# Kernel tuning notes

Measured on AMD Instinct MI355X. Metric: run time of the kernel, lower is better.

## Reference

```python
import jax, jax.numpy as jnp
import numpy as np

B, L, D, K = 1024, 50, 128, 20
NI, NL, NT = 100000, 10000, 2000  # items, locs, times


def _emb(k, n, d):
    e = jax.random.normal(k, (n, d), dtype=jnp.float32) * 0.02
    return e.at[0].set(0.0)  # padding_idx=0


def setup_inputs() -> dict:
    key = jax.random.key(0)
    ks = jax.random.split(key, 40)
    inp = {}
    inp['item'] = jax.random.randint(ks[0], (B, L), 0, NI)
    inp['locs'] = jax.random.randint(ks[1], (B,), 0, NL)
    inp['times'] = jax.random.randint(ks[2], (B,), 0, NT)
    inp['session_emb'] = jax.random.normal(ks[3], (B, 1, D), dtype=jnp.float32)
    # embedding tables
    inp['loc_emb'] = _emb(ks[4], NL, D)
    inp['time_emb'] = _emb(ks[5], NT, D)
    inp['item_emb'] = _emb(ks[6], NI, D)
    # sampled fixed-fanout neighbor tables Hg[edge]['neighbor']
    inp['nb_IL'] = jax.random.randint(ks[7], (NL, K), 0, NI)   # item neighbors of locs
    inp['nb_TL'] = jax.random.randint(ks[8], (NL, K), 0, NT)   # time neighbors of locs
    inp['nb_IT'] = jax.random.randint(ks[9], (NT, K), 0, NI)   # item neighbors of times
    inp['nb_LT'] = jax.random.randint(ks[10], (NT, K), 0, NL)  # loc neighbors of times
    inp['nb_II'] = jax.random.randint(ks[11], (NI, K), 0, NI)  # item neighbors of items
    inp['nb_LI'] = jax.random.randint(ks[12], (NI, K), 0, NL)  # loc neighbors of items
    inp['nb_TI'] = jax.random.randint(ks[13], (NI, K), 0, NT)  # time neighbors of items
    # 7 HeteAggregator params: Linear(2D -> D) + ReLU
    s = 1.0 / np.sqrt(2 * D)
    names = ['IL', 'TL', 'IT', 'LT', 'II', 'LI', 'TI']
    for i, nm in enumerate(names):
        inp['W_' + nm] = jax.random.uniform(ks[14 + i], (2 * D, D), jnp.float32, -s, s)
        inp['b_' + nm] = jnp.zeros((D,), jnp.float32)
    # 3 SemanticAttention params: Linear(D->D,bias)+tanh, Linear(D->1,no bias)
    s2 = 1.0 / np.sqrt(D)
    for i, nm in enumerate(['l', 't', 'i']):
        inp['Ws_' + nm] = jax.random.uniform(ks[24 + 3 * i], (D, D), jnp.float32, -s2, s2)
        inp['bs_' + nm] = jnp.zeros((D,), jnp.float32)
        inp['q_' + nm] = jax.random.uniform(ks[25 + 3 * i], (D, 1), jnp.float32, -s2, s2)
    return inp


def hete_agg(h_self, h_neigh, W, b):
    # h_self: [N, D]; h_neigh: [N, K, D] -> mean-aggregate, concat, linear, relu
    agg = h_neigh.mean(axis=1)
    return jax.nn.relu(jnp.concatenate([h_self, agg], axis=-1) @ W + b)


def sem_att(z, Ws, bs, q):
    # HAN-style semantic attention. z: [N, M, D]
    w = jnp.tanh(z @ Ws + bs) @ q          # [N, M, 1]
    beta = jax.nn.softmax(w.mean(axis=0), axis=0)  # [M, 1]
    return (beta[None] * z).sum(axis=1)    # [N, D]


def reference(item, locs, times, session_emb,
              loc_emb, time_emb, item_emb,
              nb_IL, nb_TL, nb_IT, nb_LT, nb_II, nb_LI, nb_TI,
              W_IL, b_IL, W_TL, b_TL, W_IT, b_IT, W_LT, b_LT,
              W_II, b_II, W_LI, b_LI, W_TI, b_TI,
              Ws_l, bs_l, q_l, Ws_t, bs_t, q_t, Ws_i, bs_i, q_i):
    iids = item.reshape(-1)  # [B*L]
    h_l_IL = hete_agg(loc_emb[locs], item_emb[nb_IL[locs]], W_IL, b_IL)
    h_l_TL = hete_agg(loc_emb[locs], time_emb[nb_TL[locs]], W_TL, b_TL)
    h_t_IT = hete_agg(time_emb[times], item_emb[nb_IT[times]], W_IT, b_IT)
    h_t_LT = hete_agg(time_emb[times], loc_emb[nb_LT[times]], W_LT, b_LT)
    h_i_II = hete_agg(item_emb[iids], item_emb[nb_II[iids]], W_II, b_II)
    h_i_LI = hete_agg(item_emb[iids], loc_emb[nb_LI[iids]], W_LI, b_LI)
    h_i_TI = hete_agg(item_emb[iids], time_emb[nb_TI[iids]], W_TI, b_TI)
    h_s = session_emb.squeeze(1)  # [B, D]
    h_l_stack = jnp.stack([h_l_IL, h_l_TL, h_s], axis=1)
    h_t_stack = jnp.stack([h_t_IT, h_t_LT, h_s], axis=1)
    h_i_stack = jnp.stack([h_i_II, h_i_TI, h_i_LI], axis=1)
    h_items = sem_att(h_i_stack, Ws_i, bs_i, q_i)
    h_locs = sem_att(h_l_stack, Ws_l, bs_l, q_l)
    h_times = sem_att(h_t_stack, Ws_t, bs_t, q_t)
    return (h_items, h_locs, h_times)
```

## Files before the change

kernel.cpp:

```cpp
#include <hip/hip_runtime.h>
#include <hip/hip_fp16.h>

#define DD 128
#define KK 20
#define TRR 32
#define NT 512

typedef unsigned int uint_t;
typedef unsigned short ushort_t;
typedef unsigned char uchar_t;
typedef _Float16 f16x8 __attribute__((ext_vector_type(8)));
typedef _Float16 f16x2 __attribute__((ext_vector_type(2)));
typedef __fp16 h16x2 __attribute__((ext_vector_type(2)));
typedef float f32x4 __attribute__((ext_vector_type(4)));
typedef float f32x2 __attribute__((ext_vector_type(2)));

union UH { __half h; ushort_t s; };
union UF { f16x2 v[4]; uint4 u4; };
union CV { h16x2 a; f16x2 b; };

#if __has_builtin(__builtin_amdgcn_cvt_scalef32_pk_f16_fp8)
#define HAVE_SCALEF32 1
#endif

__device__ __forceinline__ float fast_tanh(float x) {
  const float e = __expf(2.f * x);
  return 1.f - 2.f / (e + 1.f);
}

__device__ __forceinline__ UF f8cvt(const uint2 v) {
  UF r;
#ifdef HAVE_SCALEF32
  r.v[0] = __builtin_amdgcn_cvt_scalef32_pk_f16_fp8(v.x, 1.0f, false);
  r.v[1] = __builtin_amdgcn_cvt_scalef32_pk_f16_fp8(v.x, 1.0f, true);
  r.v[2] = __builtin_amdgcn_cvt_scalef32_pk_f16_fp8(v.y, 1.0f, false);
  r.v[3] = __builtin_amdgcn_cvt_scalef32_pk_f16_fp8(v.y, 1.0f, true);
#else
  f32x2 p;
  CV c;
  p = __builtin_amdgcn_cvt_pk_f32_fp8(v.x, false);
  c.a = __builtin_amdgcn_cvt_pkrtz(p[0], p[1]); r.v[0] = c.b;
  p = __builtin_amdgcn_cvt_pk_f32_fp8(v.x, true);
  c.a = __builtin_amdgcn_cvt_pkrtz(p[0], p[1]); r.v[1] = c.b;
  p = __builtin_amdgcn_cvt_pk_f32_fp8(v.y, false);
  c.a = __builtin_amdgcn_cvt_pkrtz(p[0], p[1]); r.v[2] = c.b;
  p = __builtin_amdgcn_cvt_pk_f32_fp8(v.y, true);
  c.a = __builtin_amdgcn_cvt_pkrtz(p[0], p[1]); r.v[3] = c.b;
#endif
  return r;
}

__device__ __forceinline__ void f8acc(f16x2* a, const uint2 v) {
  const UF r = f8cvt(v);
  a[0] += r.v[0]; a[1] += r.v[1]; a[2] += r.v[2]; a[3] += r.v[3];
}

__device__ __forceinline__ void f8acc16(f16x2* a, const uint4 v) {
  uint2 lo; lo.x = v.x; lo.y = v.y;
  uint2 hi; hi.x = v.z; hi.y = v.w;
  f8acc(a, lo);
  f8acc(a + 4, hi);
}

__device__ __forceinline__ uint4 packf32x8(const float4 v0, const float4 v1) {
  UH h0, h1, h2, h3, h4, h5, h6, h7;
  h0.h = __float2half_rn(v0.x); h1.h = __float2half_rn(v0.y);
  h2.h = __float2half_rn(v0.z); h3.h = __float2half_rn(v0.w);
  h4.h = __float2half_rn(v1.x); h5.h = __float2half_rn(v1.y);
  h6.h = __float2half_rn(v1.z); h7.h = __float2half_rn(v1.w);
  uint4 o;
  o.x = (uint_t)h0.s | ((uint_t)h1.s << 16);
  o.y = (uint_t)h2.s | ((uint_t)h3.s << 16);
  o.z = (uint_t)h4.s | ((uint_t)h5.s << 16);
  o.w = (uint_t)h6.s | ((uint_t)h7.s << 16);
  return o;
}

struct CvtArgs {
  const float* item; const float* loc; const float* timet;
  uchar_t* dst8;
};

__global__ __launch_bounds__(256)
void k_cvt3(CvtArgs a) {
  const int t = blockIdx.x * blockDim.x + threadIdx.x;
  const float* src;
  if (t < 1600000) src = a.item + (size_t)t * 8;
  else if (t < 1760000) src = a.loc + ((size_t)t - 1600000) * 8;
  else src = a.timet + ((size_t)t - 1760000) * 8;
  const float4* ip = reinterpret_cast<const float4*>(src);
  const float4 x = ip[0], y = ip[1];
  uint_t p0 = __builtin_amdgcn_cvt_pk_fp8_f32(x.x, x.y, 0u, false);
  p0 = __builtin_amdgcn_cvt_pk_fp8_f32(x.z, x.w, p0, true);
  uint_t p1 = __builtin_amdgcn_cvt_pk_fp8_f32(y.x, y.y, 0u, false);
  p1 = __builtin_amdgcn_cvt_pk_fp8_f32(y.z, y.w, p1, true);
  uint2 q; q.x = p0; q.y = p1;
  reinterpret_cast<uint2*>(a.dst8)[t] = q;
}

struct PackArgs {
  const float* src[10];
  ushort_t* dst;
};

__global__ __launch_bounds__(256)
void k_pack10(PackArgs a) {
  const int b = blockIdx.x, tid = threadIdx.x;
  int job, tin;
  size_t doff;
  if (b < 112) {
    job = b >> 4; tin = ((b & 15) << 8) | tid;
    doff = (size_t)job * 32768;
  } else {
    job = 7 + ((b - 112) >> 3); tin = (((b - 112) & 7) << 8) | tid;
    doff = 7ull * 32768 + (size_t)(job - 7) * 16384;
  }
  const float* W = a.src[job];
  const int l = tin & 63;
  const int ktnt = tin >> 6;
  const int nt = ktnt & 7;
  const int kt = ktnt >> 3;
  const int col = nt * 16 + (l & 15);
  const int kb = kt * 32 + ((l >> 4) << 3);
  UH h[8];
#pragma unroll
  for (int j = 0; j < 8; ++j) h[j].h = __float2half_rn(W[(size_t)(kb + j) * DD + col]);
  uint4 o;
  o.x = (uint_t)h[0].s | ((uint_t)h[1].s << 16);
  o.y = (uint_t)h[2].s | ((uint_t)h[3].s << 16);
  o.z = (uint_t)h[4].s | ((uint_t)h[5].s << 16);
  o.w = (uint_t)h[6].s | ((uint_t)h[7].s << 16);
  *reinterpret_cast<uint4*>(a.dst + doff + (size_t)ktnt * 512 + l * 8) = o;
}

struct MegaArgs {
  const int* item_idx; const float* item_f;
  const int* nbI[3]; const uchar_t* embI[3]; const ushort_t* pWI[3]; const float* bI[3];
  const ushort_t* pWsI; const float* bsI; const float* qI;
  ushort_t* hI; float* wsumI;
  const int* sidx[2]; const float* st_f[2];
  const int* nbS[2][2]; const uchar_t* embS[2][2];
  const ushort_t* pWS[2][2]; const float* bS[2][2];
  const ushort_t* pWsS[2]; const float* bsS[2]; const float* qS[2];
  const float* session;
  ushort_t* hS[2]; float* wsumS[2];
};

__global__ __launch_bounds__(NT, 6)
void k_mega(MegaArgs a) {
  __shared__ int ids[TRR];
  __shared__ int nidx[3][TRR][KK];
  __shared__ __align__(16) ushort_t xs[TRR][4 * DD + 8];
  __shared__ float red[8][TRR];

  const int tid = threadIdx.x;
  const int l = tid & 63;
  const int w = tid >> 6;
  const int bid = blockIdx.x;

  const bool isS = bid < 64;
  const int g = isS ? (bid >> 5) : 0;
  const int bl = isS ? (bid & 31) : (bid - 64);
  const int n0 = bl * TRR;

  const int* sidx;
  const float* selfF;
  const int* nb_[3];
  const uchar_t* emb_[3];
  const ushort_t* pW_[3];
  const float* bias_[3];
  const ushort_t* pws; const float* bss; const float* qp;
  ushort_t* hd; float* wbase;
  if (!isS) {
    sidx = a.item_idx; selfF = a.item_f;
    nb_[0] = a.nbI[0]; nb_[1] = a.nbI[1]; nb_[2] = a.nbI[2];
    emb_[0] = a.embI[0]; emb_[1] = a.embI[1]; emb_[2] = a.embI[2];
    pW_[0] = a.pWI[0]; pW_[1] = a.pWI[1]; pW_[2] = a.pWI[2];
    bias_[0] = a.bI[0]; bias_[1] = a.bI[1]; bias_[2] = a.bI[2];
    pws = a.pWsI; bss = a.bsI; qp = a.qI;
    hd = a.hI; wbase = a.wsumI;
  } else if (g == 0) {
    sidx = a.sidx[0]; selfF = a.st_f[0];
    nb_[0] = a.nbS[0][0]; nb_[1] = a.nbS[0][1]; nb_[2] = nullptr;
    emb_[0] = a.embS[0][0]; emb_[1] = a.embS[0][1]; emb_[2] = nullptr;
    pW_[0] = a.pWS[0][0]; pW_[1] = a.pWS[0][1]; pW_[2] = nullptr;
    bias_[0] = a.bS[0][0]; bias_[1] = a.bS[0][1]; bias_[2] = nullptr;
    pws = a.pWsS[0]; bss = a.bsS[0]; qp = a.qS[0];
    hd = a.hS[0]; wbase = a.wsumS[0];
  } else {
    sidx = a.sidx[1]; selfF = a.st_f[1];
    nb_[0] = a.nbS[1][0]; nb_[1] = a.nbS[1][1]; nb_[2] = nullptr;
    emb_[0] = a.embS[1][0]; emb_[1] = a.embS[1][1]; emb_[2] = nullptr;
    pW_[0] = a.pWS[1][0]; pW_[1] = a.pWS[1][1]; pW_[2] = nullptr;
    bias_[0] = a.bS[1][0]; bias_[1] = a.bS[1][1]; bias_[2] = nullptr;
    pws = a.pWsS[1]; bss = a.bsS[1]; qp = a.qS[1];
    hd = a.hS[1]; wbase = a.wsumS[1];
  }

  if (tid < TRR) ids[tid] = sidx[n0 + tid];
  __syncthreads();

  const int gr = tid >> 4;
  const int gsl = tid & 15;

#pragma unroll
  for (int e = 0; e < 3; ++e) {
    if (nb_[e]) {
      for (int t = tid; t < TRR * KK; t += NT) {
        const int rr = t / KK, kk = t - rr * KK;
        nidx[e][rr][kk] = nb_[e][(size_t)ids[rr] * KK + kk];
      }
    }
  }
  {
    const float* sp = selfF + ((size_t)ids[gr] << 7) + gsl * 8;
    const float4 v0 = *reinterpret_cast<const float4*>(sp);
    const float4 v1 = *reinterpret_cast<const float4*>(sp + 4);
    *reinterpret_cast<uint4*>(&xs[gr][gsl * 8]) = packf32x8(v0, v1);
  }
  __syncthreads();

  const _Float16 sch = (_Float16)(1.f / KK);
  const f16x2 scv = (f16x2){sch, sch};
  const int lcol = l & 15;
  const int g8 = (l >> 4) << 3;
  const int col0 = w * 16 + lcol;

  if (!isS) {
    if (tid < 256) {
      const int r = tid >> 3;
      const int sl = tid & 7;
      f16x2 a0[8], a1[8], a2[8];
#pragma unroll
      for (int i = 0; i < 8; ++i) { a0[i] = (f16x2)0; a1[i] = (f16x2)0; a2[i] = (f16x2)0; }
#pragma unroll
      for (int kb = 0; kb < KK; kb += 2) {
        uint4 u0[2], u1[2], u2[2];
#pragma unroll
        for (int j = 0; j < 2; ++j)
          u0[j] = *reinterpret_cast<const uint4*>(
              emb_[0] + ((size_t)nidx[0][r][kb + j] << 7) + sl * 16);
#pragma unroll
        for (int j = 0; j < 2; ++j)
          u1[j] = *reinterpret_cast<const uint4*>(
              emb_[1] + ((size_t)nidx[1][r][kb + j] << 7) + sl * 16);
#pragma unroll
        for (int j = 0; j < 2; ++j)
          u2[j] = *reinterpret_cast<const uint4*>(
              emb_[2] + ((size_t)nidx[2][r][kb + j] << 7) + sl * 16);
#pragma unroll
        for (int j = 0; j < 2; ++j) {
          f8acc16(a0, u0[j]); f8acc16(a1, u1[j]); f8acc16(a2, u2[j]);
        }
      }
#pragma unroll
      for (int i = 0; i < 8; ++i) { a0[i] *= scv; a1[i] *= scv; a2[i] *= scv; }
      UF P;
      P.v[0] = a0[0]; P.v[1] = a0[1]; P.v[2] = a0[2]; P.v[3] = a0[3];
      *reinterpret_cast<uint4*>(&xs[r][1 * DD + sl * 16]) = P.u4;
      P.v[0] = a0[4]; P.v[1] = a0[5]; P.v[2] = a0[6]; P.v[3] = a0[7];
      *reinterpret_cast<uint4*>(&xs[r][1 * DD + sl * 16 + 8]) = P.u4;
      P.v[0] = a1[0]; P.v[1] = a1[1]; P.v[2] = a1[2]; P.v[3] = a1[3];
      *reinterpret_cast<uint4*>(&xs[r][2 * DD + sl * 16]) = P.u4;
      P.v[0] = a1[4]; P.v[1] = a1[5]; P.v[2] = a1[6]; P.v[3] = a1[7];
      *reinterpret_cast<uint4*>(&xs[r][2 * DD + sl * 16 + 8]) = P.u4;
      P.v[0] = a2[0]; P.v[1] = a2[1]; P.v[2] = a2[2]; P.v[3] = a2[3];
      *reinterpret_cast<uint4*>(&xs[r][3 * DD + sl * 16]) = P.u4;
      P.v[0] = a2[4]; P.v[1] = a2[5]; P.v[2] = a2[6]; P.v[3] = a2[7];
      *reinterpret_cast<uint4*>(&xs[r][3 * DD + sl * 16 + 8]) = P.u4;
    }
  } else {
    UF A0, A1;
#pragma unroll
    for (int i = 0; i < 4; ++i) { A0.v[i] = (f16x2)0; A1.v[i] = (f16x2)0; }
#pragma unroll
    for (int kb = 0; kb < KK; kb += 5) {
      uint2 u0[5], u1[5];
#pragma unroll
      for (int j = 0; j < 5; ++j)
        u0[j] = *reinterpret_cast<const uint2*>(
            emb_[0] + ((size_t)nidx[0][gr][kb + j] << 7) + gsl * 8);
#pragma unroll
      for (int j = 0; j < 5; ++j)
        u1[j] = *reinterpret_cast<const uint2*>(
            emb_[1] + ((size_t)nidx[1][gr][kb + j] << 7) + gsl * 8);
#pragma unroll
      for (int j = 0; j < 5; ++j) { f8acc(A0.v, u0[j]); f8acc(A1.v, u1[j]); }
    }
#pragma unroll
    for (int i = 0; i < 4; ++i) { A0.v[i] *= scv; A1.v[i] *= scv; }
    *reinterpret_cast<uint4*>(&xs[gr][1 * DD + gsl * 8]) = A0.u4;
    *reinterpret_cast<uint4*>(&xs[gr][2 * DD + gsl * 8]) = A1.u4;
    const float* srow = a.session + (size_t)(n0 + gr) * DD + gsl * 8;
    const float4 v0 = *reinterpret_cast<const float4*>(srow);
    const float4 v1 = *reinterpret_cast<const float4*>(srow + 4);
    const uint4 o = packf32x8(v0, v1);
    *reinterpret_cast<uint4*>(&xs[gr][3 * DD + gsl * 8]) = o;
    *reinterpret_cast<uint4*>(hd + (size_t)(n0 + gr) * 3 * DD + 2 * DD + gsl * 8) = o;
  }
  __syncthreads();

#pragma unroll
  for (int e = 0; e < 3; ++e) {
    const bool full = (!isS) || (e < 2);
    if (full) {
      const ushort_t* pWp = pW_[e];
      const float* bp = bias_[e];
      f32x4 acc0, acc1;
      {
        const float b0 = bp[col0];
        acc0 = (f32x4){b0, b0, b0, b0};
        acc1 = acc0;
#pragma unroll
        for (int kt = 0; kt < 8; ++kt) {
          const int xcol = (kt < 4) ? (kt * 32 + g8) : (e * DD + kt * 32 + g8);
          const f16x8 Aa = *reinterpret_cast<const f16x8*>((const void*)&xs[lcol][xcol]);
          const f16x8 Ab = *reinterpret_cast<const f16x8*>((const void*)&xs[16 + lcol][xcol]);
          const f16x8 B = *reinterpret_cast<const f16x8*>(
              (const void*)(pWp + ((size_t)(kt * 8 + w) * 512) + l * 8));
          acc0 = __builtin_amdgcn_mfma_f32_16x16x32_f16(Aa, B, acc0, 0, 0, 0);
          acc1 = __builtin_amdgcn_mfma_f32_16x16x32_f16(Ab, B, acc1, 0, 0, 0);
        }
#pragma unroll
        for (int j = 0; j < 4; ++j) {
          acc0[j] = fmaxf(acc0[j], 0.f);
          acc1[j] = fmaxf(acc1[j], 0.f);
        }
      }
      __syncthreads();
      {
        const int rbase = (l >> 4) << 2;
#pragma unroll
        for (int j = 0; j < 4; ++j) {
          const int r0 = rbase + j, r1 = 16 + rbase + j;
          UH h0, h1;
          h0.h = __float2half_rn(acc0[j]);
          h1.h = __float2half_rn(acc1[j]);
          hd[(size_t)(n0 + r0) * 3 * DD + e * DD + col0] = h0.s;
          hd[(size_t)(n0 + r1) * 3 * DD + e * DD + col0] = h1.s;
          xs[r0][(e + 1) * DD + col0] = h0.s;
          xs[r1][(e + 1) * DD + col0] = h1.s;
        }
      }
      __syncthreads();
    }
    {
      const float b0 = bss[col0];
      f32x4 s0 = (f32x4){b0, b0, b0, b0};
      f32x4 s1 = s0;
#pragma unroll
      for (int kt = 0; kt < 4; ++kt) {
        const f16x8 Aa = *reinterpret_cast<const f16x8*>(
            (const void*)&xs[lcol][(e + 1) * DD + kt * 32 + g8]);
        const f16x8 Ab = *reinterpret_cast<const f16x8*>(
            (const void*)&xs[16 + lcol][(e + 1) * DD + kt * 32 + g8]);
        const f16x8 B = *reinterpret_cast<const f16x8*>(
            (const void*)(pws + ((size_t)(kt * 8 + w) * 512) + l * 8));
        s0 = __builtin_amdgcn_mfma_f32_16x16x32_f16(Aa, B, s0, 0, 0, 0);
        s1 = __builtin_amdgcn_mfma_f32_16x16x32_f16(Ab, B, s1, 0, 0, 0);
      }
      const float q0 = qp[col0];
      float p0[4], p1[4];
#pragma unroll
      for (int j = 0; j < 4; ++j) {
        p0[j] = fast_tanh(s0[j]) * q0;
        p1[j] = fast_tanh(s1[j]) * q0;
      }
#pragma unroll
      for (int off = 1; off < 16; off <<= 1) {
#pragma unroll
        for (int j = 0; j < 4; ++j) {
          p0[j] += __shfl_xor(p0[j], off, 64);
          p1[j] += __shfl_xor(p1[j], off, 64);
        }
      }
      if (lcol == 0) {
        const int rbase = (l >> 4) << 2;
#pragma unroll
        for (int j = 0; j < 4; ++j) {
          red[w][rbase + j] = p0[j];
          red[w][16 + rbase + j] = p1[j];
        }
      }
    }
    __syncthreads();
    if (tid < TRR) {
      float s = 0.f;
#pragma unroll
      for (int ww = 0; ww < 8; ++ww) s += red[ww][tid];
#pragma unroll
      for (int off = 1; off < 32; off <<= 1) s += __shfl_xor(s, off, 64);
      if (tid == 0) atomicAdd(&wbase[(bl & 63) * 4 + e], s);
    }
    __syncthreads();
  }
}

__global__ void k_beta(const float* __restrict__ wsum, float* __restrict__ beta) {
  if (threadIdx.x == 0 && blockIdx.x == 0) {
    const float invN[3] = {1.f / 51200.f, 1.f / 1024.f, 1.f / 1024.f};
    for (int g = 0; g < 3; ++g) {
      float s0 = 0.f, s1 = 0.f, s2 = 0.f;
      for (int bkt = 0; bkt < 64; ++bkt) {
        s0 += wsum[g * 256 + bkt * 4 + 0];
        s1 += wsum[g * 256 + bkt * 4 + 1];
        s2 += wsum[g * 256 + bkt * 4 + 2];
      }
      s0 *= invN[g]; s1 *= invN[g]; s2 *= invN[g];
      const float mx = fmaxf(s0, fmaxf(s1, s2));
      const float e0 = expf(s0 - mx), e1 = expf(s1 - mx), e2 = expf(s2 - mx);
      const float inv = 1.f / (e0 + e1 + e2);
      beta[g * 4 + 0] = e0 * inv;
      beta[g * 4 + 1] = e1 * inv;
      beta[g * 4 + 2] = e2 * inv;
    }
  }
}

__global__ __launch_bounds__(256)
void k_out(const ushort_t* __restrict__ h, const float* __restrict__ beta,
           float* __restrict__ out) {
  const int t = blockIdx.x * blockDim.x + threadIdx.x;
  const int row = t >> 5;
  const int c0 = (t & 31) * 4;
  const int g = (row < 51200) ? 0 : ((row < 52224) ? 1 : 2);
  const float* bt = beta + g * 4;
  const size_t base = (size_t)row * 3 * DD + c0;
  const ushort4 ha = *reinterpret_cast<const ushort4*>(&h[base]);
  const ushort4 hb = *reinterpret_cast<const ushort4*>(&h[base + DD]);
  const ushort4 hc = *reinterpret_cast<const ushort4*>(&h[base + 2 * DD]);
  UH u;
  float4 o;
  float va, vb, vc;
  u.s = ha.x; va = __half2float(u.h); u.s = hb.x; vb = __half2float(u.h);
  u.s = hc.x; vc = __half2float(u.h);
  o.x = bt[0] * va + bt[1] * vb + bt[2] * vc;
  u.s = ha.y; va = __half2float(u.h); u.s = hb.y; vb = __half2float(u.h);
  u.s = hc.y; vc = __half2float(u.h);
  o.y = bt[0] * va + bt[1] * vb + bt[2] * vc;
  u.s = ha.z; va = __half2float(u.h); u.s = hb.z; vb = __half2float(u.h);
  u.s = hc.z; vc = __half2float(u.h);
  o.z = bt[0] * va + bt[1] * vb + bt[2] * vc;
  u.s = ha.w; va = __half2float(u.h); u.s = hb.w; vb = __half2float(u.h);
  u.s = hc.w; vc = __half2float(u.h);
  o.w = bt[0] * va + bt[1] * vb + bt[2] * vc;
  *reinterpret_cast<float4*>(&out[(size_t)row * DD + c0]) = o;
}


extern "C" void kernel_launch(void* const* d_in, const int* in_sizes, int n_in,
                              void* d_out, int out_size, void* d_ws, size_t ws_size,
                              hipStream_t stream) {
  const int*   item     = (const int*)  d_in[0];
  const int*   locs     = (const int*)  d_in[1];
  const int*   times    = (const int*)  d_in[2];
  const float* session  = (const float*)d_in[3];
  const float* loc_emb  = (const float*)d_in[4];
  const float* time_emb = (const float*)d_in[5];
  const float* item_emb = (const float*)d_in[6];
  const int* nb_IL = (const int*)d_in[7];
  const int* nb_TL = (const int*)d_in[8];
  const int* nb_IT = (const int*)d_in[9];
  const int* nb_LT = (const int*)d_in[10];
  const int* nb_II = (const int*)d_in[11];
  const int* nb_LI = (const int*)d_in[12];
  const int* nb_TI = (const int*)d_in[13];
  const float* W_IL = (const float*)d_in[14]; const float* b_IL = (const float*)d_in[15];
  const float* W_TL = (const float*)d_in[16]; const float* b_TL = (const float*)d_in[17];
  const float* W_IT = (const float*)d_in[18]; const float* b_IT = (const float*)d_in[19];
  const float* W_LT = (const float*)d_in[20]; const float* b_LT = (const float*)d_in[21];
  const float* W_II = (const float*)d_in[22]; const float* b_II = (const float*)d_in[23];
  const float* W_LI = (const float*)d_in[24]; const float* b_LI = (const float*)d_in[25];
  const float* W_TI = (const float*)d_in[26]; const float* b_TI = (const float*)d_in[27];
  const float* Ws_l = (const float*)d_in[28]; const float* bs_l = (const float*)d_in[29];
  const float* q_l  = (const float*)d_in[30];
  const float* Ws_t = (const float*)d_in[31]; const float* bs_t = (const float*)d_in[32];
  const float* q_t  = (const float*)d_in[33];
  const float* Ws_i = (const float*)d_in[34]; const float* bs_i = (const float*)d_in[35];
  const float* q_i  = (const float*)d_in[36];

  float* outp = (float*)d_out;

  char* wsb = (char*)d_ws;
  float* wsum  = (float*)wsb;
  float* betap = (float*)wsb + 1024;
  ushort_t* pk = (ushort_t*)(wsb + 16384);
  ushort_t* pk_II = pk;
  ushort_t* pk_TI = pk_II + 32768;
  ushort_t* pk_LI = pk_TI + 32768;
  ushort_t* pk_IL = pk_LI + 32768;
  ushort_t* pk_TL = pk_IL + 32768;
  ushort_t* pk_IT = pk_TL + 32768;
  ushort_t* pk_LT = pk_IT + 32768;
  ushort_t* pk_Wi = pk_LT + 32768;
  ushort_t* pk_Wl = pk_Wi + 16384;
  ushort_t* pk_Wt = pk_Wl + 16384;
  ushort_t* hbuf  = pk_Wt + 16384;
  uchar_t* item_8 = (uchar_t*)(hbuf + (size_t)53248 * 3 * DD);
  uchar_t* loc_8  = item_8 + (size_t)100000 * DD;
  uchar_t* time_8 = loc_8 + (size_t)10000 * DD;

  (void)hipMemsetAsync(d_ws, 0, 16384, stream);

  CvtArgs ca;
  ca.item = item_emb; ca.loc = loc_emb; ca.timet = time_emb;
  ca.dst8 = item_8;
  k_cvt3<<<dim3(7000), dim3(256), 0, stream>>>(ca);

  PackArgs pa;
  pa.src[0] = W_II; pa.src[1] = W_TI; pa.src[2] = W_LI;
  pa.src[3] = W_IL; pa.src[4] = W_TL; pa.src[5] = W_IT; pa.src[6] = W_LT;
  pa.src[7] = Ws_i; pa.src[8] = Ws_l; pa.src[9] = Ws_t;
  pa.dst = pk;
  k_pack10<<<dim3(136), dim3(256), 0, stream>>>(pa);

  ushort_t* h_items = hbuf;
  ushort_t* h_locs  = hbuf + (size_t)51200 * 3 * DD;
  ushort_t* h_times = hbuf + (size_t)52224 * 3 * DD;

  MegaArgs ma;
  ma.item_idx = item; ma.item_f = item_emb;
  ma.nbI[0] = nb_II; ma.nbI[1] = nb_TI; ma.nbI[2] = nb_LI;
  ma.embI[0] = item_8; ma.embI[1] = time_8; ma.embI[2] = loc_8;
  ma.pWI[0] = pk_II; ma.pWI[1] = pk_TI; ma.pWI[2] = pk_LI;
  ma.bI[0] = b_II; ma.bI[1] = b_TI; ma.bI[2] = b_LI;
  ma.pWsI = pk_Wi; ma.bsI = bs_i; ma.qI = q_i;
  ma.hI = h_items; ma.wsumI = wsum + 0;
  ma.sidx[0] = locs;  ma.sidx[1] = times;
  ma.st_f[0] = loc_emb; ma.st_f[1] = time_emb;
  ma.nbS[0][0] = nb_IL; ma.nbS[0][1] = nb_TL;
  ma.nbS[1][0] = nb_IT; ma.nbS[1][1] = nb_LT;
  ma.embS[0][0] = item_8; ma.embS[0][1] = time_8;
  ma.embS[1][0] = item_8; ma.embS[1][1] = loc_8;
  ma.pWS[0][0] = pk_IL; ma.pWS[0][1] = pk_TL;
  ma.pWS[1][0] = pk_IT; ma.pWS[1][1] = pk_LT;
  ma.bS[0][0] = b_IL; ma.bS[0][1] = b_TL;
  ma.bS[1][0] = b_IT; ma.bS[1][1] = b_LT;
  ma.pWsS[0] = pk_Wl; ma.pWsS[1] = pk_Wt;
  ma.bsS[0] = bs_l; ma.bsS[1] = bs_t;
  ma.qS[0] = q_l; ma.qS[1] = q_t;
  ma.session = session;
  ma.hS[0] = h_locs; ma.hS[1] = h_times;
  ma.wsumS[0] = wsum + 256; ma.wsumS[1] = wsum + 512;
  k_mega<<<dim3(64 + 51200 / TRR), dim3(NT), 0, stream>>>(ma);

  k_beta<<<dim3(1), dim3(64), 0, stream>>>(wsum, betap);
  k_out<<<dim3((53248 * 32) / 256), dim3(256), 0, stream>>>(hbuf, betap, outp);
}
```

Baseline: 118.2 us.

## Split item aggregation across blocks per edge type and shrink session tiles

The fused kernel now gives each item-tile/edge-type pair its own 256-thread block, for three times as many item blocks. Previously one 512-thread block handled all three edge types in sequence with barriers between them. Each wave now computes two 16-column MFMA tiles, and the location/time blocks process 16 rows instead of 32, doubling their block count. The intent is more independent blocks to hide gather latency and a shorter barrier chain per block. The cost is loading item ids and self features three times, plus more atomics into the attention-score buckets.

Result: slower. 124.2 us (+5.1%).

```diff
diff --git a/kernel.cpp b/kernel.cpp
--- a/kernel.cpp
+++ b/kernel.cpp
@@ -3,8 +3,7 @@
 
 #define DD 128
 #define KK 20
-#define TRR 32
-#define NT 512
+#define NT 256
 
 typedef unsigned int uint_t;
 typedef unsigned short ushort_t;
@@ -148,223 +147,149 @@
 
 __global__ __launch_bounds__(NT, 6)
 void k_mega(MegaArgs a) {
-  __shared__ int ids[TRR];
-  __shared__ int nidx[3][TRR][KK];
-  __shared__ __align__(16) ushort_t xs[TRR][4 * DD + 8];
-  __shared__ float red[8][TRR];
+  __shared__ int ids[32];
+  __shared__ int nidx[640];
+  __shared__ __align__(16) ushort_t xs[8320];
+  __shared__ float red[128];
 
   const int tid = threadIdx.x;
   const int l = tid & 63;
   const int w = tid >> 6;
   const int bid = blockIdx.x;
-
-  const bool isS = bid < 64;
-  const int g = isS ? (bid >> 5) : 0;
-  const int bl = isS ? (bid & 31) : (bid - 64);
-  const int n0 = bl * TRR;
-
-  const int* sidx;
-  const float* selfF;
-  const int* nb_[3];
-  const uchar_t* emb_[3];
-  const ushort_t* pW_[3];
-  const float* bias_[3];
-  const ushort_t* pws; const float* bss; const float* qp;
-  ushort_t* hd; float* wbase;
-  if (!isS) {
-    sidx = a.item_idx; selfF = a.item_f;
-    nb_[0] = a.nbI[0]; nb_[1] = a.nbI[1]; nb_[2] = a.nbI[2];
-    emb_[0] = a.embI[0]; emb_[1] = a.embI[1]; emb_[2] = a.embI[2];
-    pW_[0] = a.pWI[0]; pW_[1] = a.pWI[1]; pW_[2] = a.pWI[2];
-    bias_[0] = a.bI[0]; bias_[1] = a.bI[1]; bias_[2] = a.bI[2];
-    pws = a.pWsI; bss = a.bsI; qp = a.qI;
-    hd = a.hI; wbase = a.wsumI;
-  } else if (g == 0) {
-    sidx = a.sidx[0]; selfF = a.st_f[0];
-    nb_[0] = a.nbS[0][0]; nb_[1] = a.nbS[0][1]; nb_[2] = nullptr;
-    emb_[0] = a.embS[0][0]; emb_[1] = a.embS[0][1]; emb_[2] = nullptr;
-    pW_[0] = a.pWS[0][0]; pW_[1] = a.pWS[0][1]; pW_[2] = nullptr;
-    bias_[0] = a.bS[0][0]; bias_[1] = a.bS[0][1]; bias_[2] = nullptr;
-    pws = a.pWsS[0]; bss = a.bsS[0]; qp = a.qS[0];
-    hd = a.hS[0]; wbase = a.wsumS[0];
-  } else {
-    sidx = a.sidx[1]; selfF = a.st_f[1];
-    nb_[0] = a.nbS[1][0]; nb_[1] = a.nbS[1][1]; nb_[2] = nullptr;
-    emb_[0] = a.embS[1][0]; emb_[1] = a.embS[1][1]; emb_[2] = nullptr;
-    pW_[0] = a.pWS[1][0]; pW_[1] = a.pWS[1][1]; pW_[2] = nullptr;
-    bias_[0] = a.bS[1][0]; bias_[1] = a.bS[1][1]; bias_[2] = nullptr;
-    pws = a.pWsS[1]; bss = a.bsS[1]; qp = a.qS[1];
-    hd = a.hS[1]; wbase = a.wsumS[1];
-  }
-
-  if (tid < TRR) ids[tid] = sidx[n0 + tid];
-  __syncthreads();
-
-  const int gr = tid >> 4;
-  const int gsl = tid & 15;
-
-#pragma unroll
-  for (int e = 0; e < 3; ++e) {
-    if (nb_[e]) {
-      for (int t = tid; t < TRR * KK; t += NT) {
-        const int rr = t / KK, kk = t - rr * KK;
-        nidx[e][rr][kk] = nb_[e][(size_t)ids[rr] * KK + kk];
-      }
-    }
-  }
-  {
-    const float* sp = selfF + ((size_t)ids[gr] << 7) + gsl * 8;
-    const float4 v0 = *reinterpret_cast<const float4*>(sp);
-    const float4 v1 = *reinterpret_cast<const float4*>(sp + 4);
-    *reinterpret_cast<uint4*>(&xs[gr][gsl * 8]) = packf32x8(v0, v1);
-  }
-  __syncthreads();
-
+  const int lcol = l & 15;
+  const int g8 = (l >> 4) << 3;
+  const int nt0 = 2 * w;
+  const int col0 = nt0 * 16 + lcol;
+  const int col1 = col0 + 16;
   const _Float16 sch = (_Float16)(1.f / KK);
   const f16x2 scv = (f16x2){sch, sch};
-  const int lcol = l & 15;
-  const int g8 = (l >> 4) << 3;
-  const int col0 = w * 16 + lcol;
-
-  if (!isS) {
-    if (tid < 256) {
-      const int r = tid >> 3;
-      const int sl = tid & 7;
-      f16x2 a0[8], a1[8], a2[8];
-#pragma unroll
-      for (int i = 0; i < 8; ++i) { a0[i] = (f16x2)0; a1[i] = (f16x2)0; a2[i] = (f16x2)0; }
-#pragma unroll
-      for (int kb = 0; kb < KK; kb += 2) {
-        uint4 u0[2], u1[2], u2[2];
-#pragma unroll
-        for (int j = 0; j < 2; ++j)
-          u0[j] = *reinterpret_cast<const uint4*>(
-              emb_[0] + ((size_t)nidx[0][r][kb + j] << 7) + sl * 16);
-#pragma unroll
-        for (int j = 0; j < 2; ++j)
-          u1[j] = *reinterpret_cast<const uint4*>(
-              emb_[1] + ((size_t)nidx[1][r][kb + j] << 7) + sl * 16);
-#pragma unroll
-        for (int j = 0; j < 2; ++j)
-          u2[j] = *reinterpret_cast<const uint4*>(
-              emb_[2] + ((size_t)nidx[2][r][kb + j] << 7) + sl * 16);
-#pragma unroll
-        for (int j = 0; j < 2; ++j) {
-          f8acc16(a0, u0[j]); f8acc16(a1, u1[j]); f8acc16(a2, u2[j]);
-        }
-      }
-#pragma unroll
-      for (int i = 0; i < 8; ++i) { a0[i] *= scv; a1[i] *= scv; a2[i] *= scv; }
+
+  if (bid >= 128) {
+    const int t = bid - 128;
+    const int e = t % 3;
+    const int tile = t / 3;
+    const int n0 = tile * 32;
+    const int* nb = a.nbI[e];
+    const uchar_t* emb = a.embI[e];
+    const ushort_t* pW = a.pWI[e];
+    const float* bias = a.bI[e];
+
+    if (tid < 32) ids[tid] = a.item_idx[n0 + tid];
+    __syncthreads();
+
+    for (int i = tid; i < 640; i += NT) {
+      const int rr = i / KK, kk = i - rr * KK;
+      nidx[i] = nb[(size_t)ids[rr] * KK + kk];
+    }
+    {
+      const int r = tid >> 3, sl = tid & 7;
+      const float* sp = a.item_f + ((size_t)ids[r] << 7) + sl * 16;
+      const float4 v0 = *reinterpret_cast<const float4*>(sp);
+      const float4 v1 = *reinterpret_cast<const float4*>(sp + 4);
+      const float4 v2 = *reinterpret_cast<const float4*>(sp + 8);
+      const float4 v3 = *reinterpret_cast<const float4*>(sp + 12);
+      *reinterpret_cast<uint4*>(&xs[r * 260 + sl * 16]) = packf32x8(v0, v1);
+      *reinterpret_cast<uint4*>(&xs[r * 260 + sl * 16 + 8]) = packf32x8(v2, v3);
+    }
+    __syncthreads();
+
+    {
+      const int r = tid >> 3, sl = tid & 7;
+      f16x2 acc[8];
+#pragma unroll
+      for (int i = 0; i < 8; ++i) acc[i] = (f16x2)0;
+#pragma unroll
+      for (int kb = 0; kb < KK; kb += 4) {
+        uint4 u[4];
+#pragma unroll
+        for (int j = 0; j < 4; ++j)
+          u[j] = *reinterpret_cast<const uint4*>(
+              emb + ((size_t)nidx[r * KK + kb + j] << 7) + sl * 16);
+#pragma unroll
+        for (int j = 0; j < 4; ++j) f8acc16(acc, u[j]);
+      }
+#pragma unroll
+      for (int i = 0; i < 8; ++i) acc[i] *= scv;
       UF P;
-      P.v[0] = a0[0]; P.v[1] = a0[1]; P.v[2] = a0[2]; P.v[3] = a0[3];
-      *reinterpret_cast<uint4*>(&xs[r][1 * DD + sl * 16]) = P.u4;
-      P.v[0] = a0[4]; P.v[1] = a0[5]; P.v[2] = a0[6]; P.v[3] = a0[7];
-      *reinterpret_cast<uint4*>(&xs[r][1 * DD + sl * 16 + 8]) = P.u4;
-      P.v[0] = a1[0]; P.v[1] = a1[1]; P.v[2] = a1[2]; P.v[3] = a1[3];
-      *reinterpret_cast<uint4*>(&xs[r][2 * DD + sl * 16]) = P.u4;
-      P.v[0] = a1[4]; P.v[1] = a1[5]; P.v[2] = a1[6]; P.v[3] = a1[7];
-      *reinterpret_cast<uint4*>(&xs[r][2 * DD + sl * 16 + 8]) = P.u4;
-      P.v[0] = a2[0]; P.v[1] = a2[1]; P.v[2] = a2[2]; P.v[3] = a2[3];
-      *reinterpret_cast<uint4*>(&xs[r][3 * DD + sl * 16]) = P.u4;
-      P.v[0] = a2[4]; P.v[1] = a2[5]; P.v[2] = a2[6]; P.v[3] = a2[7];
-      *reinterpret_cast<uint4*>(&xs[r][3 * DD + sl * 16 + 8]) = P.u4;
-    }
-  } else {
-    UF A0, A1;
-#pragma unroll
-    for (int i = 0; i < 4; ++i) { A0.v[i] = (f16x2)0; A1.v[i] = (f16x2)0; }
-#pragma unroll
-    for (int kb = 0; kb < KK; kb += 5) {
-      uint2 u0[5], u1[5];
-#pragma unroll
-      for (int j = 0; j < 5; ++j)
-        u0[j] = *reinterpret_cast<const uint2*>(
-            emb_[0] + ((size_t)nidx[0][gr][kb + j] << 7) + gsl * 8);
-#pragma unroll
-      for (int j = 0; j < 5; ++j)
-        u1[j] = *reinterpret_cast<const uint2*>(
-            emb_[1] + ((size_t)nidx[1][gr][kb + j] << 7) + gsl * 8);
-#pragma unroll
-      for (int j = 0; j < 5; ++j) { f8acc(A0.v, u0[j]); f8acc(A1.v, u1[j]); }
-    }
-#pragma unroll
-    for (int i = 0; i < 4; ++i) { A0.v[i] *= scv; A1.v[i] *= scv; }
-    *reinterpret_cast<uint4*>(&xs[gr][1 * DD + gsl * 8]) = A0.u4;
-    *reinterpret_cast<uint4*>(&xs[gr][2 * DD + gsl * 8]) = A1.u4;
-    const float* srow = a.session + (size_t)(n0 + gr) * DD + gsl * 8;
-    const float4 v0 = *reinterpret_cast<const float4*>(srow);
-    const float4 v1 = *reinterpret_cast<const float4*>(srow + 4);
-    const uint4 o = packf32x8(v0, v1);
-    *reinterpret_cast<uint4*>(&xs[gr][3 * DD + gsl * 8]) = o;
-    *reinterpret_cast<uint4*>(hd + (size_t)(n0 + gr) * 3 * DD + 2 * DD + gsl * 8) = o;
-  }
-  __syncthreads();
-
-#pragma unroll
-  for (int e = 0; e < 3; ++e) {
-    const bool full = (!isS) || (e < 2);
-    if (full) {
-      const ushort_t* pWp = pW_[e];
-      const float* bp = bias_[e];
-      f32x4 acc0, acc1;
-      {
-        const float b0 = bp[col0];
-        acc0 = (f32x4){b0, b0, b0, b0};
-        acc1 = acc0;
-#pragma unroll
-        for (int kt = 0; kt < 8; ++kt) {
-          const int xcol = (kt < 4) ? (kt * 32 + g8) : (e * DD + kt * 32 + g8);
-          const f16x8 Aa = *reinterpret_cast<const f16x8*>((const void*)&xs[lcol][xcol]);
-          const f16x8 Ab = *reinterpret_cast<const f16x8*>((const void*)&xs[16 + lcol][xcol]);
-          const f16x8 B = *reinterpret_cast<const f16x8*>(
-              (const void*)(pWp + ((size_t)(kt * 8 + w) * 512) + l * 8));
-          acc0 = __builtin_amdgcn_mfma_f32_16x16x32_f16(Aa, B, acc0, 0, 0, 0);
-          acc1 = __builtin_amdgcn_mfma_f32_16x16x32_f16(Ab, B, acc1, 0, 0, 0);
-        }
-#pragma unroll
-        for (int j = 0; j < 4; ++j) {
-          acc0[j] = fmaxf(acc0[j], 0.f);
-          acc1[j] = fmaxf(acc1[j], 0.f);
-        }
-      }
-      __syncthreads();
-      {
-        const int rbase = (l >> 4) << 2;
-#pragma unroll
-        for (int j = 0; j < 4; ++j) {
-          const int r0 = rbase + j, r1 = 16 + rbase + j;
-          UH h0, h1;
-          h0.h = __float2half_rn(acc0[j]);
-          h1.h = __float2half_rn(acc1[j]);
-          hd[(size_t)(n0 + r0) * 3 * DD + e * DD + col0] = h0.s;
-          hd[(size_t)(n0 + r1) * 3 * DD + e * DD + col0] = h1.s;
-          xs[r0][(e + 1) * DD + col0] = h0.s;
-          xs[r1][(e + 1) * DD + col0] = h1.s;
-        }
-      }
-      __syncthreads();
-    }
+      P.v[0] = acc[0]; P.v[1] = acc[1]; P.v[2] = acc[2]; P.v[3] = acc[3];
+      *reinterpret_cast<uint4*>(&xs[r * 260 + 128 + sl * 16]) = P.u4;
+      P.v[0] = acc[4]; P.v[1] = acc[5]; P.v[2] = acc[6]; P.v[3] = acc[7];
+      *reinterpret_cast<uint4*>(&xs[r * 260 + 128 + sl * 16 + 8]) = P.u4;
+    }
+    __syncthreads();
+
+    f32x4 a00, a01, a10, a11;
     {
-      const float b0 = bss[col0];
-      f32x4 s0 = (f32x4){b0, b0, b0, b0};
-      f32x4 s1 = s0;
+      const float b0 = bias[col0], b1 = bias[col1];
+      a00 = (f32x4){b0, b0, b0, b0}; a01 = (f32x4){b1, b1, b1, b1};
+      a10 = a00; a11 = a01;
+#pragma unroll
+      for (int kt = 0; kt < 8; ++kt) {
+        const int xcol = kt * 32 + g8;
+        const f16x8 Aa = *reinterpret_cast<const f16x8*>((const void*)&xs[lcol * 260 + xcol]);
+        const f16x8 Ab = *reinterpret_cast<const f16x8*>((const void*)&xs[(16 + lcol) * 260 + xcol]);
+        const f16x8 B0 = *reinterpret_cast<const f16x8*>(
+            (const void*)(pW + ((size_t)(kt * 8 + nt0) * 512) + l * 8));
+        const f16x8 B1 = *reinterpret_cast<const f16x8*>(
+            (const void*)(pW + ((size_t)(kt * 8 + nt0 + 1) * 512) + l * 8));
+        a00 = __builtin_amdgcn_mfma_f32_16x16x32_f16(Aa, B0, a00, 0, 0, 0);
+        a01 = __builtin_amdgcn_mfma_f32_16x16x32_f16(Aa, B1, a01, 0, 0, 0);
+        a10 = __builtin_amdgcn_mfma_f32_16x16x32_f16(Ab, B0, a10, 0, 0, 0);
+        a11 = __builtin_amdgcn_mfma_f32_16x16x32_f16(Ab, B1, a11, 0, 0, 0);
+      }
+#pragma unroll
+      for (int j = 0; j < 4; ++j) {
+        a00[j] = fmaxf(a00[j], 0.f); a01[j] = fmaxf(a01[j], 0.f);
+        a10[j] = fmaxf(a10[j], 0.f); a11[j] = fmaxf(a11[j], 0.f);
+      }
+    }
+    __syncthreads();
+    {
+      const int rbase = (l >> 4) << 2;
+#pragma unroll
+      for (int j = 0; j < 4; ++j) {
+        const int r0 = rbase + j, r1 = 16 + rbase + j;
+        UH h00, h01, h10, h11;
+        h00.h = __float2half_rn(a00[j]); h01.h = __float2half_rn(a01[j]);
+        h10.h = __float2half_rn(a10[j]); h11.h = __float2half_rn(a11[j]);
+        a.hI[(size_t)(n0 + r0) * 3 * DD + e * DD + col0] = h00.s;
+        a.hI[(size_t)(n0 + r0) * 3 * DD + e * DD + col1] = h01.s;
+        a.hI[(size_t)(n0 + r1) * 3 * DD + e * DD + col0] = h10.s;
+        a.hI[(size_t)(n0 + r1) * 3 * DD + e * DD + col1] = h11.s;
+        xs[r0 * 260 + 128 + col0] = h00.s;
+        xs[r0 * 260 + 128 + col1] = h01.s;
+        xs[r1 * 260 + 128 + col0] = h10.s;
+        xs[r1 * 260 + 128 + col1] = h11.s;
+      }
+    }
+    __syncthreads();
+
+    {
+      const float b0 = a.bsI[col0], b1 = a.bsI[col1];
+      f32x4 s00 = (f32x4){b0, b0, b0, b0};
+      f32x4 s01 = (f32x4){b1, b1, b1, b1};
+      f32x4 s10 = s00, s11 = s01;
 #pragma unroll
       for (int kt = 0; kt < 4; ++kt) {
         const f16x8 Aa = *reinterpret_cast<const f16x8*>(
-            (const void*)&xs[lcol][(e + 1) * DD + kt * 32 + g8]);
+            (const void*)&xs[lcol * 260 + 128 + kt * 32 + g8]);
         const f16x8 Ab = *reinterpret_cast<const f16x8*>(
-            (const void*)&xs[16 + lcol][(e + 1) * DD + kt * 32 + g8]);
-        const f16x8 B = *reinterpret_cast<const f16x8*>(
-            (const void*)(pws + ((size_t)(kt * 8 + w) * 512) + l * 8));
-        s0 = __builtin_amdgcn_mfma_f32_16x16x32_f16(Aa, B, s0, 0, 0, 0);
-        s1 = __builtin_amdgcn_mfma_f32_16x16x32_f16(Ab, B, s1, 0, 0, 0);
-      }
-      const float q0 = qp[col0];
+            (const void*)&xs[(16 + lcol) * 260 + 128 + kt * 32 + g8]);
+        const f16x8 B0 = *reinterpret_cast<const f16x8*>(
+            (const void*)(a.pWsI + ((size_t)(kt * 8 + nt0) * 512) + l * 8));
+        const f16x8 B1 = *reinterpret_cast<const f16x8*>(
+            (const void*)(a.pWsI + ((size_t)(kt * 8 + nt0 + 1) * 512) + l * 8));
+        s00 = __builtin_amdgcn_mfma_f32_16x16x32_f16(Aa, B0, s00, 0, 0, 0);
+        s01 = __builtin_amdgcn_mfma_f32_16x16x32_f16(Aa, B1, s01, 0, 0, 0);
+        s10 = __builtin_amdgcn_mfma_f32_16x16x32_f16(Ab, B0, s10, 0, 0, 0);
+        s11 = __builtin_amdgcn_mfma_f32_16x16x32_f16(Ab, B1, s11, 0, 0, 0);
+      }
+      const float q0 = a.qI[col0], q1 = a.qI[col1];
       float p0[4], p1[4];
 #pragma unroll
       for (int j = 0; j < 4; ++j) {
-        p0[j] = fast_tanh(s0[j]) * q0;
-        p1[j] = fast_tanh(s1[j]) * q0;
+        p0[j] = fast_tanh(s00[j]) * q0 + fast_tanh(s01[j]) * q1;
+        p1[j] = fast_tanh(s10[j]) * q0 + fast_tanh(s11[j]) * q1;
       }
 #pragma unroll
       for (int off = 1; off < 16; off <<= 1) {
@@ -378,21 +303,160 @@
         const int rbase = (l >> 4) << 2;
 #pragma unroll
         for (int j = 0; j < 4; ++j) {
-          red[w][rbase + j] = p0[j];
-          red[w][16 + rbase + j] = p1[j];
+          red[w * 32 + rbase + j] = p0[j];
+          red[w * 32 + 16 + rbase + j] = p1[j];
         }
       }
     }
     __syncthreads();
-    if (tid < TRR) {
-      float s = 0.f;
-#pragma unroll
-      for (int ww = 0; ww < 8; ++ww) s += red[ww][tid];
+    if (tid < 32) {
+      float s = red[tid] + red[32 + tid] + red[64 + tid] + red[96 + tid];
 #pragma unroll
       for (int off = 1; off < 32; off <<= 1) s += __shfl_xor(s, off, 64);
-      if (tid == 0) atomicAdd(&wbase[(bl & 63) * 4 + e], s);
-    }
-    __syncthreads();
+      if (tid == 0) atomicAdd(&a.wsumI[(tile & 63) * 4 + e], s);
+    }
+  } else {
+    const int g = bid >> 6;
+    const int bl = bid & 63;
+    const int n0 = bl * 16;
+    const int gr = tid >> 4;
+    const int gsl = tid & 15;
+    ushort_t* hd = a.hS[g];
+    const ushort_t* pws = a.pWsS[g];
+    const float* bss = a.bsS[g];
+    const float* qp = a.qS[g];
+
+    if (tid < 16) ids[tid] = a.sidx[g][n0 + tid];
+    __syncthreads();
+    for (int i = tid; i < 640; i += NT) {
+      const int e2 = i / 320;
+      const int r2 = (i - e2 * 320) / KK;
+      const int k2 = i - e2 * 320 - r2 * KK;
+      nidx[i] = a.nbS[g][e2][(size_t)ids[r2] * KK + k2];
+    }
+    {
+      const float* sp = a.st_f[g] + ((size_t)ids[gr] << 7) + gsl * 8;
+      const float4 v0 = *reinterpret_cast<const float4*>(sp);
+      const float4 v1 = *reinterpret_cast<const float4*>(sp + 4);
+      *reinterpret_cast<uint4*>(&xs[gr * 520 + gsl * 8]) = packf32x8(v0, v1);
+    }
+    __syncthreads();
+
+    {
+      UF A0, A1;
+#pragma unroll
+      for (int i = 0; i < 4; ++i) { A0.v[i] = (f16x2)0; A1.v[i] = (f16x2)0; }
+#pragma unroll
+      for (int kb = 0; kb < KK; kb += 5) {
+        uint2 u0[5], u1[5];
+#pragma unroll
+        for (int j = 0; j < 5; ++j)
+          u0[j] = *reinterpret_cast<const uint2*>(
+              a.embS[g][0] + ((size_t)nidx[gr * KK + kb + j] << 7) + gsl * 8);
+#pragma unroll
+        for (int j = 0; j < 5; ++j)
+          u1[j] = *reinterpret_cast<const uint2*>(
+              a.embS[g][1] + ((size_t)nidx[320 + gr * KK + kb + j] << 7) + gsl * 8);
+#pragma unroll
+        for (int j = 0; j < 5; ++j) { f8acc(A0.v, u0[j]); f8acc(A1.v, u1[j]); }
+      }
+#pragma unroll
+      for (int i = 0; i < 4; ++i) { A0.v[i] *= scv; A1.v[i] *= scv; }
+      *reinterpret_cast<uint4*>(&xs[gr * 520 + 128 + gsl * 8]) = A0.u4;
+      *reinterpret_cast<uint4*>(&xs[gr * 520 + 256 + gsl * 8]) = A1.u4;
+      const float* srow = a.session + (size_t)(n0 + gr) * DD + gsl * 8;
+      const float4 v0 = *reinterpret_cast<const float4*>(srow);
+      const float4 v1 = *reinterpret_cast<const float4*>(srow + 4);
+      const uint4 o = packf32x8(v0, v1);
+      *reinterpret_cast<uint4*>(&xs[gr * 520 + 384 + gsl * 8]) = o;
+      *reinterpret_cast<uint4*>(hd + (size_t)(n0 + gr) * 3 * DD + 2 * DD + gsl * 8) = o;
+    }
+    __syncthreads();
+
+#pragma unroll
+    for (int e = 0; e < 3; ++e) {
+      if (e < 2) {
+        const ushort_t* pW = a.pWS[g][e];
+        const float* bp = a.bS[g][e];
+        f32x4 acc0, acc1;
+        {
+          const float b0 = bp[col0], b1 = bp[col1];
+          acc0 = (f32x4){b0, b0, b0, b0};
+          acc1 = (f32x4){b1, b1, b1, b1};
+#pragma unroll
+          for (int kt = 0; kt < 8; ++kt) {
+            const int xcol = (kt < 4) ? (kt * 32 + g8) : (e * DD + kt * 32 + g8);
+            const f16x8 Aa = *reinterpret_cast<const f16x8*>((const void*)&xs[lcol * 520 + xcol]);
+            const f16x8 B0 = *reinterpret_cast<const f16x8*>(
+                (const void*)(pW + ((size_t)(kt * 8 + nt0) * 512) + l * 8));
+            const f16x8 B1 = *reinterpret_cast<const f16x8*>(
+                (const void*)(pW + ((size_t)(kt * 8 + nt0 + 1) * 512) + l * 8));
+            acc0 = __builtin_amdgcn_mfma_f32_16x16x32_f16(Aa, B0, acc0, 0, 0, 0);
+            acc1 = __builtin_amdgcn_mfma_f32_16x16x32_f16(Aa, B1, acc1, 0, 0, 0);
+          }
+#pragma unroll
+          for (int j = 0; j < 4; ++j) {
+            acc0[j] = fmaxf(acc0[j], 0.f);
+            acc1[j] = fmaxf(acc1[j], 0.f);
+          }
+        }
+        __syncthreads();
+        {
+          const int rbase = (l >> 4) << 2;
+#pragma unroll
+          for (int j = 0; j < 4; ++j) {
+            const int r0 = rbase + j;
+            UH h0, h1;
+            h0.h = __float2half_rn(acc0[j]);
+            h1.h = __float2half_rn(acc1[j]);
+            hd[(size_t)(n0 + r0) * 3 * DD + e * DD + col0] = h0.s;
+            hd[(size_t)(n0 + r0) * 3 * DD + e * DD + col1] = h1.s;
+            xs[r0 * 520 + (e + 1) * DD + col0] = h0.s;
+            xs[r0 * 520 + (e + 1) * DD + col1] = h1.s;
+          }
+        }
+        __syncthreads();
+      }
+      {
+        const float b0 = bss[col0], b1 = bss[col1];
+        f32x4 s0 = (f32x4){b0, b0, b0, b0};
+        f32x4 s1 = (f32x4){b1, b1, b1, b1};
+#pragma unroll
+        for (int kt = 0; kt < 4; ++kt) {
+          const f16x8 Aa = *reinterpret_cast<const f16x8*>(
+              (const void*)&xs[lcol * 520 + (e + 1) * DD + kt * 32 + g8]);
+          const f16x8 B0 = *reinterpret_cast<const f16x8*>(
+              (const void*)(pws + ((size_t)(kt * 8 + nt0) * 512) + l * 8));
+          const f16x8 B1 = *reinterpret_cast<const f16x8*>(
+              (const void*)(pws + ((size_t)(kt * 8 + nt0 + 1) * 512) + l * 8));
+          s0 = __builtin_amdgcn_mfma_f32_16x16x32_f16(Aa, B0, s0, 0, 0, 0);
+          s1 = __builtin_amdgcn_mfma_f32_16x16x32_f16(Aa, B1, s1, 0, 0, 0);
+        }
+        const float q0 = qp[col0], q1 = qp[col1];
+        float p0[4];
+#pragma unroll
+        for (int j = 0; j < 4; ++j)
+          p0[j] = fast_tanh(s0[j]) * q0 + fast_tanh(s1[j]) * q1;
+#pragma unroll
+        for (int off = 1; off < 16; off <<= 1) {
+#pragma unroll
+          for (int j = 0; j < 4; ++j) p0[j] += __shfl_xor(p0[j], off, 64);
+        }
+        if (lcol == 0) {
+          const int rbase = (l >> 4) << 2;
+#pragma unroll
+          for (int j = 0; j < 4; ++j) red[w * 32 + rbase + j] = p0[j];
+        }
+      }
+      __syncthreads();
+      if (tid < 16) {
+        float s = red[tid] + red[32 + tid] + red[64 + tid] + red[96 + tid];
+#pragma unroll
+        for (int off = 1; off < 16; off <<= 1) s += __shfl_xor(s, off, 64);
+        if (tid == 0) atomicAdd(&a.wsumS[g][(bl & 63) * 4 + e], s);
+      }
+      __syncthreads();
+    }
   }
 }
 
@@ -542,7 +606,7 @@
   ma.session = session;
   ma.hS[0] = h_locs; ma.hS[1] = h_times;
   ma.wsumS[0] = wsum + 256; ma.wsumS[1] = wsum + 512;
-  k_mega<<<dim3(64 + 51200 / TRR), dim3(NT), 0, stream>>>(ma);
+  k_mega<<<dim3(128 + 4800), dim3(NT), 0, stream>>>(ma);
 
   k_beta<<<dim3(1), dim3(64), 0, stream>>>(wsum, betap);
   k_out<<<dim3((53248 * 32) / 256), dim3(256), 0, stream>>>(hbuf, betap, outp);
```
